# Optimization experiments

Measured on AMD Instinct MI355X. Metric: run time of the kernel, lower is better.

Reference implementation:

```python
import jax, jax.numpy as jnp
import numpy as np

N, E, F_IN, NCLS, H = 50000, 800000, 128, 10, 64


def setup_inputs() -> dict:
    key = jax.random.key(0)
    ks = jax.random.split(key, 24)
    p = lambda k, shp: (jax.random.normal(k, shp, dtype=jnp.float32) * 0.1)
    inp = {
        'x': jax.random.normal(ks[0], (N, F_IN), dtype=jnp.float32),
        'edge_index': jax.random.randint(ks[1], (2, E), 0, N, dtype=jnp.int64),
        'gcn1_W': p(ks[2], (F_IN, 128)), 'gcn1_b': p(ks[3], (128,)),
        'gcn2_W': p(ks[4], (128, 64)),  'gcn2_b': p(ks[5], (64,)),
        'gcn3_W': p(ks[6], (64, 32)),   'gcn3_b': p(ks[7], (32,)),
        'gat_W': p(ks[8], (32, 32)), 'gat_a_src': p(ks[9], (32,)),
        'gat_a_dst': p(ks[10], (32,)), 'gat_b': p(ks[11], (32,)),
        'lstm_Wih_f': p(ks[12], (4 * H, 32)), 'lstm_bih_f': p(ks[13], (4 * H,)), 'lstm_bhh_f': p(ks[14], (4 * H,)),
        'lstm_Wih_b': p(ks[15], (4 * H, 32)), 'lstm_bih_b': p(ks[16], (4 * H,)), 'lstm_bhh_b': p(ks[17], (4 * H,)),
        'bn_gamma': jnp.ones((2 * H,), jnp.float32), 'bn_beta': jnp.zeros((2 * H,), jnp.float32),
        'fc_W': p(ks[18], (NCLS, 2 * H)), 'fc_b': p(ks[19], (NCLS,)),
    }
    return inp


def _forward(x, edge_index, gcn1_W, gcn1_b, gcn2_W, gcn2_b, gcn3_W, gcn3_b,
             gat_W, gat_a_src, gat_a_dst, gat_b,
             lstm_Wih_f, lstm_bih_f, lstm_bhh_f, lstm_Wih_b, lstm_bih_b, lstm_bhh_b,
             bn_gamma, bn_beta, fc_W, fc_b):
    n = x.shape[0]
    loop = jnp.arange(n)
    row = jnp.concatenate([edge_index[0], loop])  # source nodes (+ self loops)
    col = jnp.concatenate([edge_index[1], loop])  # target nodes
    deg = jax.ops.segment_sum(jnp.ones_like(col, dtype=x.dtype), col, num_segments=n)
    dis = jax.lax.rsqrt(jnp.maximum(deg, 1e-12))  # deg >= 1 due to self loops
    norm = dis[row] * dis[col]

    def gcn(h, W, b):
        h = h @ W
        return jax.ops.segment_sum(h[row] * norm[:, None], col, num_segments=n) + b

    h = jax.nn.relu(gcn(x, gcn1_W, gcn1_b))
    h = jax.nn.relu(gcn(h, gcn2_W, gcn2_b))
    h = gcn(h, gcn3_W, gcn3_b)

    # GAT (1 head), self loops already in row/col, softmax over incoming edges per target
    g = h @ gat_W
    e = jax.nn.leaky_relu((g @ gat_a_src)[row] + (g @ gat_a_dst)[col], negative_slope=0.2)
    m = jax.ops.segment_max(e, col, num_segments=n)
    ee = jnp.exp(e - m[col])
    att = ee / jax.ops.segment_sum(ee, col, num_segments=n)[col]
    h = jax.ops.segment_sum(g[row] * att[:, None], col, num_segments=n) + gat_b
    h = jax.nn.relu(h)

    # bidirectional LSTM with seq_len=1, h0=c0=0 -> single cell step per direction
    def lstm_dir(xx, Wih, bih, bhh):
        gt = xx @ Wih.T + bih + bhh
        i, f, c, o = jnp.split(gt, 4, axis=-1)  # torch gate order i,f,g,o
        return jax.nn.sigmoid(o) * jnp.tanh(jax.nn.sigmoid(i) * jnp.tanh(c))

    r = jnp.concatenate([lstm_dir(h, lstm_Wih_f, lstm_bih_f, lstm_bhh_f),
                         lstm_dir(h, lstm_Wih_b, lstm_bih_b, lstm_bhh_b)], axis=-1)
    # eval mode: dropout = identity; BatchNorm1d with running_mean=0, running_var=1
    r = r * (bn_gamma / jnp.sqrt(jnp.float32(1.0 + 1e-5))) + bn_beta
    return r @ fc_W.T + fc_b


def reference(x, edge_index, gcn1_W, gcn1_b, gcn2_W, gcn2_b, gcn3_W, gcn3_b,
              gat_W, gat_a_src, gat_a_dst, gat_b,
              lstm_Wih_f, lstm_bih_f, lstm_bhh_f, lstm_Wih_b, lstm_bih_b, lstm_bhh_b,
              bn_gamma, bn_beta, fc_W, fc_b):
    return _forward(x, edge_index, gcn1_W, gcn1_b, gcn2_W, gcn2_b, gcn3_W, gcn3_b,
                    gat_W, gat_a_src, gat_a_dst, gat_b,
                    lstm_Wih_f, lstm_bih_f, lstm_bhh_f, lstm_Wih_b, lstm_bih_b, lstm_bhh_b,
                    bn_gamma, bn_beta, fc_W, fc_b)
```

## Files before the change

### kernel.cpp

```cpp
#include <hip/hip_runtime.h>
#include <hip/hip_bf16.h>
#include <math.h>

typedef __hip_bfloat16 bf16;

#define NN 50000
#define EE 800000
#define EPB 4096
#define NBK 196
#define BCAP 6144

__device__ __forceinline__ float b2f(bf16 v) { return __bfloat162float(v); }
__device__ __forceinline__ float rcp_(float x) { return __builtin_amdgcn_rcpf(x); }
__device__ __forceinline__ float sigmoidf_(float x) { return rcp_(1.0f + __expf(-x)); }
__device__ __forceinline__ float tanhf_(float x) {
    float xx = fminf(fmaxf(x, -15.0f), 15.0f);
    float e = __expf(2.0f * xx);
    return (e - 1.0f) * rcp_(e + 1.0f);
}
__device__ __forceinline__ float leakyf_(float x) { return x > 0.0f ? x : 0.2f * x; }
__device__ __forceinline__ unsigned short f2bf(float f) {
    unsigned u = __float_as_uint(f);
    unsigned r = (u + 0x7FFFu + ((u >> 16) & 1u)) >> 16;
    return (unsigned short)r;
}
__device__ __forceinline__ unsigned pack2(float a, float b) {
    return (unsigned)f2bf(a) | ((unsigned)f2bf(b) << 16);
}
__device__ __forceinline__ float lo_(unsigned u) { return __uint_as_float(u << 16); }
__device__ __forceinline__ float hi_(unsigned u) { return __uint_as_float(u & 0xFFFF0000u); }

#define OFF_W1 0
#define OFF_B1 16384
#define OFF_W2 16512
#define OFF_B2 24704
#define OFF_W3 24768
#define OFF_B3 26816
#define OFF_GATW 26848
#define OFF_GAS 27872
#define OFF_GAD 27904
#define OFF_GAB 27936
#define OFF_WIHF 27968
#define OFF_BIHF 36160
#define OFF_BHHF 36416
#define OFF_WIHB 36672
#define OFF_BIHB 44864
#define OFF_BHHB 45120
#define OFF_GAMMA 45376
#define OFF_BETA 45504
#define OFF_FCW 45632
#define OFF_FCB 46912
#define WTOTAL 46922

struct WSrc { const void* p[20]; };

__global__ void k_detect(const unsigned short* __restrict__ xraw,
                         const unsigned int* __restrict__ eraw, int* __restrict__ flags) {
    __shared__ int f32f, i64f;
    int t = threadIdx.x;
    if (t == 0) { f32f = 0; i64f = 1; }
    __syncthreads();
    for (int i = t; i < 4096; i += 256) {
        unsigned short u = xraw[i];
        int ex = (u >> 7) & 0xFF;
        if (ex >= 0xC0) atomicOr(&f32f, 1);
        if (eraw[2 * i + 1] != 0u) atomicAnd(&i64f, 0);
    }
    __syncthreads();
    if (t == 0) { flags[0] = f32f; flags[1] = i64f; }
}

__global__ void k_cvt_w(WSrc srcs, float* __restrict__ dst, const int* __restrict__ flags,
                        int total) {
    constexpr int WOFF[21] = {OFF_W1,   OFF_B1,   OFF_W2,   OFF_B2,   OFF_W3,   OFF_B3,
                              OFF_GATW, OFF_GAS,  OFF_GAD,  OFF_GAB,  OFF_WIHF, OFF_BIHF,
                              OFF_BHHF, OFF_WIHB, OFF_BIHB, OFF_BHHB, OFF_GAMMA, OFF_BETA,
                              OFF_FCW,  OFF_FCB,  WTOTAL};
    int i = blockIdx.x * 256 + threadIdx.x;
    if (i >= total) return;
    int tn = 0;
#pragma unroll
    for (int j = 1; j < 20; ++j)
        if (i >= WOFF[j]) tn = j;
    int local = i - WOFF[tn];
    if (flags[0]) dst[i] = ((const float*)srcs.p[tn])[local];
    else dst[i] = b2f(((const bf16*)srcs.p[tn])[local]);
}

__global__ __launch_bounds__(256) void k_hist(const void* __restrict__ eraw,
                                              unsigned* __restrict__ gh,
                                              const int* __restrict__ flags) {
    __shared__ int h[256];
    int t = threadIdx.x, b = blockIdx.x;
    h[t] = 0;
    __syncthreads();
    int e0 = b * EPB;
    bool i64 = flags[1] != 0;
    for (int i = t; i < EPB; i += 256) {
        int e = e0 + i;
        if (e < EE) {
            int d = i64 ? (int)((const long long*)eraw)[EE + e] : ((const int*)eraw)[EE + e];
            d = min(max(d, 0), NN - 1);
            atomicAdd(&h[d >> 8], 1);
        }
    }
    __syncthreads();
    gh[b * 256 + t] = (unsigned)h[t];
}

__global__ __launch_bounds__(256) void k_bscan(const unsigned* __restrict__ gh,
                                               unsigned* __restrict__ gh2,
                                               int* __restrict__ bb, int* __restrict__ rptr) {
    __shared__ int s[256];
    int t = threadIdx.x;
    unsigned run = 0;
    for (int blk = 0; blk < NBK; ++blk) {
        unsigned v = gh[blk * 256 + t];
        gh2[blk * 256 + t] = run;
        run += v;
    }
    s[t] = (int)run;
    __syncthreads();
    for (int o = 1; o < 256; o <<= 1) {
        int x = (t >= o) ? s[t - o] : 0;
        __syncthreads();
        s[t] += x;
        __syncthreads();
    }
    bb[t] = s[t] - (int)run;
    if (t == 0) rptr[NN] = EE;
}

__global__ __launch_bounds__(256) void k_scatter(const void* __restrict__ eraw,
                                                 const unsigned* __restrict__ gh2,
                                                 const int* __restrict__ bb,
                                                 int2* __restrict__ ebkt,
                                                 const int* __restrict__ flags) {
    __shared__ unsigned cur[256];
    int t = threadIdx.x, b = blockIdx.x;
    cur[t] = gh2[b * 256 + t] + (unsigned)bb[t];
    __syncthreads();
    int e0 = b * EPB;
    bool i64 = flags[1] != 0;
    for (int i = t; i < EPB; i += 256) {
        int e = e0 + i;
        if (e < EE) {
            int sn, d;
            if (i64) {
                sn = (int)((const long long*)eraw)[e];
                d = (int)((const long long*)eraw)[EE + e];
            } else {
                sn = ((const int*)eraw)[e];
                d = ((const int*)eraw)[EE + e];
            }
            sn = min(max(sn, 0), NN - 1);
            d = min(max(d, 0), NN - 1);
            unsigned pos = atomicAdd(&cur[d >> 8], 1u);
            if (pos < (unsigned)EE) ebkt[pos] = make_int2(sn, d);
        }
    }
}

__global__ __launch_bounds__(256) void k_bucket_csr(const int2* __restrict__ ebkt,
                                                    const int* __restrict__ bb,
                                                    int* __restrict__ rptr,
                                                    float* __restrict__ dis,
                                                    int* __restrict__ csr_src) {
    __shared__ int hist[256];
    __shared__ int excl[256];
    __shared__ int cur[256];
    __shared__ int sorted[BCAP];
    int t = threadIdx.x, b = blockIdx.x;
    int s0 = bb[b], s1 = bb[b + 1];
    int len = min(s1 - s0, BCAP);
    hist[t] = 0;
    __syncthreads();
    for (int i = t; i < len; i += 256) atomicAdd(&hist[ebkt[s0 + i].y & 255], 1);
    __syncthreads();
    int v = hist[t];
    excl[t] = v;
    __syncthreads();
    for (int o = 1; o < 256; o <<= 1) {
        int x = (t >= o) ? excl[t - o] : 0;
        __syncthreads();
        excl[t] += x;
        __syncthreads();
    }
    int loc = excl[t] - v;
    int node = b * 256 + t;
    if (node < NN) {
        rptr[node] = s0 + loc;
        dis[node] = rsqrtf((float)(v + 1));
    }
    cur[t] = loc;
    __syncthreads();
    for (int i = t; i < len; i += 256) {
        int2 p = ebkt[s0 + i];
        int pos = atomicAdd(&cur[p.y & 255], 1);
        if (pos < BCAP) sorted[pos] = p.x;
    }
    __syncthreads();
    for (int i = t; i < len; i += 256) csr_src[s0 + i] = sorted[i];
}

template <int KIN, int KOUT, int MODE, bool SCALE>
__global__ __launch_bounds__(256) void k_tile_mm(const void* __restrict__ A,
                                                 const float* __restrict__ W,
                                                 unsigned* __restrict__ C, int n,
                                                 const int* __restrict__ flags, int want,
                                                 const float* __restrict__ dis) {
    if (want >= 0 && flags[0] != want) return;
    constexpr int BK = 32;
    constexpr int AST = BK + 4;
    constexpr int CPT = KOUT / 16;
    __shared__ float As[64 * AST];
    __shared__ float Ws[BK * KOUT];
    int t = threadIdx.x;
    int jc = t & 15;
    int ng = t >> 4;
    int base = blockIdx.x * 64;
    float acc[4][CPT];
#pragma unroll
    for (int i = 0; i < 4; ++i)
#pragma unroll
        for (int c = 0; c < CPT; ++c) acc[i][c] = 0.f;
    int snode = t >> 2;
    int gnode = min(base + snode, n - 1);
    int koff = (t & 3) * 8;
    for (int k0 = 0; k0 < KIN; k0 += BK) {
        {
            const float4* src = (const float4*)(W + k0 * KOUT);
            float4* dst = (float4*)Ws;
#pragma unroll
            for (int p = 0; p < BK * KOUT / 1024; ++p) dst[t + p * 256] = src[t + p * 256];
        }
        if (MODE == 0) {
            const unsigned* xr = (const unsigned*)A + (size_t)gnode * (KIN / 2) + (k0 + koff) / 2;
            unsigned u0 = xr[0], u1 = xr[1], u2 = xr[2], u3 = xr[3];
            float* d = As + snode * AST + koff;
            d[0] = lo_(u0); d[1] = hi_(u0);
            d[2] = lo_(u1); d[3] = hi_(u1);
            d[4] = lo_(u2); d[5] = hi_(u2);
            d[6] = lo_(u3); d[7] = hi_(u3);
        } else {
            const float4* ar = (const float4*)((const float*)A + (size_t)gnode * KIN + k0 + koff);
            float4 v0 = ar[0], v1 = ar[1];
            float4* d = (float4*)(As + snode * AST + koff);
            d[0] = v0;
            d[1] = v1;
        }
        __syncthreads();
#pragma unroll 8
        for (int k = 0; k < BK; ++k) {
            float w[CPT];
            const float* wr = Ws + k * KOUT + jc * CPT;
            if constexpr (CPT >= 4) {
#pragma unroll
                for (int c = 0; c < CPT; c += 4) {
                    float4 wv = *(const float4*)(wr + c);
                    w[c] = wv.x; w[c + 1] = wv.y; w[c + 2] = wv.z; w[c + 3] = wv.w;
                }
            } else {
                float2 wv = *(const float2*)wr;
                w[0] = wv.x; w[1] = wv.y;
            }
            float a0 = As[(ng * 4 + 0) * AST + k];
            float a1 = As[(ng * 4 + 1) * AST + k];
            float a2 = As[(ng * 4 + 2) * AST + k];
            float a3 = As[(ng * 4 + 3) * AST + k];
#pragma unroll
            for (int c = 0; c < CPT; ++c) {
                acc[0][c] += a0 * w[c];
                acc[1][c] += a1 * w[c];
                acc[2][c] += a2 * w[c];
                acc[3][c] += a3 * w[c];
            }
        }
        __syncthreads();
    }
#pragma unroll
    for (int i = 0; i < 4; ++i) {
        int node = base + ng * 4 + i;
        if (node < n) {
            float sc = SCALE ? dis[node] : 1.0f;
            unsigned* cr = C + (size_t)node * (KOUT / 2) + jc * (CPT / 2);
#pragma unroll
            for (int c = 0; c < CPT; c += 2)
                cr[c / 2] = pack2(acc[i][c] * sc, acc[i][c + 1] * sc);
        }
    }
}

template <bool RELU>
__global__ void k_agg128(const unsigned* __restrict__ t, const int* __restrict__ rptr,
                         const int* __restrict__ csr_src, const float* __restrict__ dis,
                         const float* __restrict__ bias, float* __restrict__ out, int n) {
    int wave = (blockIdx.x * blockDim.x + threadIdx.x) >> 6;
    int lane = threadIdx.x & 63;
    if (wave >= n) return;
    int dst = wave;
    float dd = dis[dst];
    float ax, ay;
    {
        unsigned u = t[(size_t)dst * 64 + lane];
        ax = lo_(u);
        ay = hi_(u);
    }
    int s = __builtin_amdgcn_readfirstlane(max(0, min(rptr[dst], EE)));
    int e = __builtin_amdgcn_readfirstlane(max(s, min(rptr[dst + 1], EE)));
    int j = s;
    for (; j + 8 <= e; j += 8) {
        int i0 = csr_src[j], i1 = csr_src[j + 1], i2 = csr_src[j + 2], i3 = csr_src[j + 3];
        int i4 = csr_src[j + 4], i5 = csr_src[j + 5], i6 = csr_src[j + 6], i7 = csr_src[j + 7];
        unsigned u0 = t[(size_t)i0 * 64 + lane], u1 = t[(size_t)i1 * 64 + lane];
        unsigned u2 = t[(size_t)i2 * 64 + lane], u3 = t[(size_t)i3 * 64 + lane];
        unsigned u4 = t[(size_t)i4 * 64 + lane], u5 = t[(size_t)i5 * 64 + lane];
        unsigned u6 = t[(size_t)i6 * 64 + lane], u7 = t[(size_t)i7 * 64 + lane];
        ax += (lo_(u0) + lo_(u1)) + (lo_(u2) + lo_(u3)) + (lo_(u4) + lo_(u5)) + (lo_(u6) + lo_(u7));
        ay += (hi_(u0) + hi_(u1)) + (hi_(u2) + hi_(u3)) + (hi_(u4) + hi_(u5)) + (hi_(u6) + hi_(u7));
    }
    for (; j + 4 <= e; j += 4) {
        int i0 = csr_src[j], i1 = csr_src[j + 1], i2 = csr_src[j + 2], i3 = csr_src[j + 3];
        unsigned u0 = t[(size_t)i0 * 64 + lane], u1 = t[(size_t)i1 * 64 + lane];
        unsigned u2 = t[(size_t)i2 * 64 + lane], u3 = t[(size_t)i3 * 64 + lane];
        ax += (lo_(u0) + lo_(u1)) + (lo_(u2) + lo_(u3));
        ay += (hi_(u0) + hi_(u1)) + (hi_(u2) + hi_(u3));
    }
    for (; j < e; ++j) {
        unsigned u0 = t[(size_t)csr_src[j] * 64 + lane];
        ax += lo_(u0);
        ay += hi_(u0);
    }
    float2 bv = *(const float2*)(bias + 2 * lane);
    float vx = ax * dd + bv.x;
    float vy = ay * dd + bv.y;
    if (RELU) { vx = fmaxf(vx, 0.f); vy = fmaxf(vy, 0.f); }
    *(float2*)(out + (size_t)dst * 128 + 2 * lane) = make_float2(vx, vy);
}

template <bool RELU>
__global__ void k_agg64(const unsigned* __restrict__ t, const int* __restrict__ rptr,
                        const int* __restrict__ csr_src, const float* __restrict__ dis,
                        const float* __restrict__ bias, float* __restrict__ out, int n) {
    int wave = (blockIdx.x * blockDim.x + threadIdx.x) >> 6;
    int lane = threadIdx.x & 63;
    if (wave >= n) return;
    int dst = wave;
    int half = lane >> 5, l32 = lane & 31;
    float dd = dis[dst];
    float ax = 0.f, ay = 0.f;
    if (!half) {
        unsigned u = t[(size_t)dst * 32 + l32];
        ax = lo_(u);
        ay = hi_(u);
    }
    int s = max(0, min(rptr[dst], EE));
    int e = max(s, min(rptr[dst + 1], EE));
    int cnt = e - s;
    int pairs = cnt >> 1;
    int p = 0;
    for (; p + 4 <= pairs; p += 4) {
        int jb = s + 2 * p + half;
        int i0 = csr_src[jb], i1 = csr_src[jb + 2], i2 = csr_src[jb + 4], i3 = csr_src[jb + 6];
        unsigned u0 = t[(size_t)i0 * 32 + l32], u1 = t[(size_t)i1 * 32 + l32];
        unsigned u2 = t[(size_t)i2 * 32 + l32], u3 = t[(size_t)i3 * 32 + l32];
        ax += (lo_(u0) + lo_(u1)) + (lo_(u2) + lo_(u3));
        ay += (hi_(u0) + hi_(u1)) + (hi_(u2) + hi_(u3));
    }
    for (; p < pairs; ++p) {
        int i0 = csr_src[s + 2 * p + half];
        unsigned u0 = t[(size_t)i0 * 32 + l32];
        ax += lo_(u0);
        ay += hi_(u0);
    }
    if ((cnt & 1) && !half) {
        unsigned u0 = t[(size_t)csr_src[e - 1] * 32 + l32];
        ax += lo_(u0);
        ay += hi_(u0);
    }
    ax += __shfl_down(ax, 32);
    ay += __shfl_down(ay, 32);
    if (!half) {
        float2 bv = *(const float2*)(bias + 2 * l32);
        float vx = ax * dd + bv.x;
        float vy = ay * dd + bv.y;
        if (RELU) { vx = fmaxf(vx, 0.f); vy = fmaxf(vy, 0.f); }
        *(float2*)(out + (size_t)dst * 64 + 2 * l32) = make_float2(vx, vy);
    }
}

template <bool RELU>
__global__ void k_agg32(const unsigned* __restrict__ t, const int* __restrict__ rptr,
                        const int* __restrict__ csr_src, const float* __restrict__ dis,
                        const float* __restrict__ bias, float* __restrict__ out, int n) {
    int wave = (blockIdx.x * blockDim.x + threadIdx.x) >> 6;
    int lane = threadIdx.x & 63;
    if (wave >= n) return;
    int dst = wave;
    int q = lane >> 4, l16 = lane & 15;
    float dd = dis[dst];
    float ax = 0.f, ay = 0.f;
    if (q == 0) {
        unsigned u = t[(size_t)dst * 16 + l16];
        ax = lo_(u);
        ay = hi_(u);
    }
    int s = max(0, min(rptr[dst], EE));
    int e = max(s, min(rptr[dst + 1], EE));
    int cnt = e - s;
    int quads = cnt >> 2;
    int p = 0;
    for (; p + 4 <= quads; p += 4) {
        int jb = s + 4 * p + q;
        int i0 = csr_src[jb], i1 = csr_src[jb + 4], i2 = csr_src[jb + 8], i3 = csr_src[jb + 12];
        unsigned u0 = t[(size_t)i0 * 16 + l16], u1 = t[(size_t)i1 * 16 + l16];
        unsigned u2 = t[(size_t)i2 * 16 + l16], u3 = t[(size_t)i3 * 16 + l16];
        ax += (lo_(u0) + lo_(u1)) + (lo_(u2) + lo_(u3));
        ay += (hi_(u0) + hi_(u1)) + (hi_(u2) + hi_(u3));
    }
    for (; p < quads; ++p) {
        int i0 = csr_src[s + 4 * p + q];
        unsigned u0 = t[(size_t)i0 * 16 + l16];
        ax += lo_(u0);
        ay += hi_(u0);
    }
    int rem = cnt - 4 * quads;
    if (q < rem) {
        unsigned u0 = t[(size_t)csr_src[s + 4 * quads + q] * 16 + l16];
        ax += lo_(u0);
        ay += hi_(u0);
    }
    ax += __shfl_down(ax, 32);
    ay += __shfl_down(ay, 32);
    ax += __shfl_down(ax, 16);
    ay += __shfl_down(ay, 16);
    if (q == 0) {
        float2 bv = *(const float2*)(bias + 2 * l16);
        float vx = ax * dd + bv.x;
        float vy = ay * dd + bv.y;
        if (RELU) { vx = fmaxf(vx, 0.f); vy = fmaxf(vy, 0.f); }
        *(float2*)(out + (size_t)dst * 32 + 2 * l16) = make_float2(vx, vy);
    }
}

__global__ void k_gat_vec(const unsigned* __restrict__ g, const float* __restrict__ a_src,
                          const float* __restrict__ a_dst, float* __restrict__ asrc,
                          float* __restrict__ adst, int n) {
    int i = blockIdx.x * 256 + threadIdx.x;
    if (i >= n) return;
    float s = 0.0f, d = 0.0f;
    const unsigned* gr = g + (size_t)i * 16;
#pragma unroll
    for (int k = 0; k < 16; ++k) {
        unsigned u = gr[k];
        float v0 = lo_(u), v1 = hi_(u);
        s += v0 * a_src[2 * k] + v1 * a_src[2 * k + 1];
        d += v0 * a_dst[2 * k] + v1 * a_dst[2 * k + 1];
    }
    asrc[i] = s;
    adst[i] = d;
}

__global__ void k_gat_agg(const unsigned* __restrict__ g, const int* __restrict__ rptr,
                          const int* __restrict__ csr_src, const float* __restrict__ asrc,
                          const float* __restrict__ adst, const float* __restrict__ gat_b,
                          float* __restrict__ out, int n) {
    int wave = (blockIdx.x * blockDim.x + threadIdx.x) >> 6;
    int lane = threadIdx.x & 63;
    if (wave >= n) return;
    int dst = wave;
    int q = lane >> 4, l16 = lane & 15;
    float ad = adst[dst];
    int s = max(0, min(rptr[dst], EE));
    int e = max(s, min(rptr[dst + 1], EE));
    float ax = 0.f, ay = 0.f, denom = 0.f;
    if (q == 0) {
        float w0 = __expf(fminf(leakyf_(asrc[dst] + ad), 80.f));
        unsigned u = g[(size_t)dst * 16 + l16];
        ax = lo_(u) * w0;
        ay = hi_(u) * w0;
        denom = w0;
    }
    int cnt = e - s;
    int quads = cnt >> 2;
    int p = 0;
    for (; p + 4 <= quads; p += 4) {
        int jb = s + 4 * p + q;
        int i0 = csr_src[jb], i1 = csr_src[jb + 4], i2 = csr_src[jb + 8], i3 = csr_src[jb + 12];
        float a0 = asrc[i0], a1 = asrc[i1], a2 = asrc[i2], a3 = asrc[i3];
        unsigned u0 = g[(size_t)i0 * 16 + l16], u1 = g[(size_t)i1 * 16 + l16];
        unsigned u2 = g[(size_t)i2 * 16 + l16], u3 = g[(size_t)i3 * 16 + l16];
        float w0 = __expf(fminf(leakyf_(a0 + ad), 80.f));
        float w1 = __expf(fminf(leakyf_(a1 + ad), 80.f));
        float w2 = __expf(fminf(leakyf_(a2 + ad), 80.f));
        float w3 = __expf(fminf(leakyf_(a3 + ad), 80.f));
        denom += (w0 + w1) + (w2 + w3);
        ax += lo_(u0) * w0 + lo_(u1) * w1 + lo_(u2) * w2 + lo_(u3) * w3;
        ay += hi_(u0) * w0 + hi_(u1) * w1 + hi_(u2) * w2 + hi_(u3) * w3;
    }
    for (; p < quads; ++p) {
        int i0 = csr_src[s + 4 * p + q];
        float wgt = __expf(fminf(leakyf_(asrc[i0] + ad), 80.f));
        unsigned u0 = g[(size_t)i0 * 16 + l16];
        denom += wgt;
        ax += lo_(u0) * wgt;
        ay += hi_(u0) * wgt;
    }
    int rem = cnt - 4 * quads;
    if (q < rem) {
        int i0 = csr_src[s + 4 * quads + q];
        float wgt = __expf(fminf(leakyf_(asrc[i0] + ad), 80.f));
        unsigned u0 = g[(size_t)i0 * 16 + l16];
        denom += wgt;
        ax += lo_(u0) * wgt;
        ay += hi_(u0) * wgt;
    }
    ax += __shfl_down(ax, 32);
    ay += __shfl_down(ay, 32);
    denom += __shfl_down(denom, 32);
    ax += __shfl_down(ax, 16);
    ay += __shfl_down(ay, 16);
    denom += __shfl_down(denom, 16);
    if (q == 0) {
        float r = rcp_(denom);
        float vx = fmaxf(ax * r + gat_b[2 * l16], 0.f);
        float vy = fmaxf(ay * r + gat_b[2 * l16 + 1], 0.f);
        *(float2*)(out + (size_t)dst * 32 + 2 * l16) = make_float2(vx, vy);
    }
}

__global__ __launch_bounds__(256) void k_lstm_fc(const float* __restrict__ h,
                                                 const float* __restrict__ wp,
                                                 void* __restrict__ out,
                                                 const int* __restrict__ flags, int n) {
    __shared__ float ps[4 * 640];
    int t = threadIdx.x;
    int nd = t & 63;
    int part = __builtin_amdgcn_readfirstlane(t >> 6);
    int dir = part >> 1, jh = part & 1;
    int base = blockIdx.x * 64;
    int node = min(base + nd, n - 1);

    float hv[32];
    {
        const float4* hr = (const float4*)(h + (size_t)node * 32);
#pragma unroll
        for (int qq = 0; qq < 8; ++qq) {
            float4 v = hr[qq];
            hv[4 * qq + 0] = v.x;
            hv[4 * qq + 1] = v.y;
            hv[4 * qq + 2] = v.z;
            hv[4 * qq + 3] = v.w;
        }
    }

    const float* W = wp + (dir ? OFF_WIHB : OFF_WIHF);
    const float* bi = wp + (dir ? OFF_BIHB : OFF_BIHF);
    const float* bh = wp + (dir ? OFF_BHHB : OFF_BHHF);
    const float* fcw = wp + OFF_FCW;
    float p10[10];
#pragma unroll
    for (int c = 0; c < 10; ++c) p10[c] = 0.f;

    int j0 = jh * 32;
#pragma unroll 2
    for (int j = j0; j < j0 + 32; ++j) {
        const float* wi = W + (size_t)j * 32;
        const float* wc = W + (size_t)(128 + j) * 32;
        const float* wo = W + (size_t)(192 + j) * 32;
        float ai = bi[j] + bh[j];
        float ac = bi[128 + j] + bh[128 + j];
        float ao = bi[192 + j] + bh[192 + j];
#pragma unroll
        for (int k = 0; k < 32; ++k) {
            float hk = hv[k];
            ai += hk * wi[k];
            ac += hk * wc[k];
            ao += hk * wo[k];
        }
        float v = sigmoidf_(ao) * tanhf_(sigmoidf_(ai) * tanhf_(ac));
        int jj = dir * 64 + j;
        float r = v * (wp[OFF_GAMMA + jj] * rsqrtf(1.0f + 1e-5f)) + wp[OFF_BETA + jj];
#pragma unroll
        for (int c = 0; c < 10; ++c) p10[c] += r * fcw[c * 128 + jj];
    }
#pragma unroll
    for (int c = 0; c < 10; ++c) ps[part * 640 + nd * 10 + c] = p10[c];
    __syncthreads();
    bool f32o = flags[0] != 0;
    for (int idx = t; idx < 640; idx += 256) {
        int gnode = base + idx / 10;
        if (gnode < n) {
            int c = idx % 10;
            float v = wp[OFF_FCB + c] + ps[idx] + ps[640 + idx] + ps[1280 + idx] + ps[1920 + idx];
            if (f32o) ((float*)out)[(size_t)base * 10 + idx] = v;
            else ((unsigned short*)out)[(size_t)base * 10 + idx] = f2bf(v);
        }
    }
}

extern "C" void kernel_launch(void* const* d_in, const int* in_sizes, int n_in,
                              void* d_out, int out_size, void* d_ws, size_t ws_size,
                              hipStream_t stream) {
    const int N = NN;

    char* w = (char*)d_ws;
    auto alloc = [&](size_t bytes) {
        void* p = (void*)w;
        w += (bytes + 255) & ~(size_t)255;
        return p;
    };
    int* flags = (int*)alloc(256);
    float* wpool = (float*)alloc((size_t)WTOTAL * 4);
    float* dis = (float*)alloc((size_t)N * 4);
    int* rptr = (int*)alloc((size_t)(N + 1) * 4);
    int* csr_src = (int*)alloc((size_t)EE * 4);
    unsigned* gh = (unsigned*)alloc((size_t)NBK * 256 * 4);
    unsigned* gh2 = (unsigned*)alloc((size_t)NBK * 256 * 4);
    int* bb = (int*)alloc(1024);
    int2* ebkt = (int2*)alloc((size_t)EE * 8);
    float* asrc = (float*)alloc((size_t)N * 4);
    float* adst = (float*)alloc((size_t)N * 4);
    unsigned* bufT = (unsigned*)alloc((size_t)N * 64 * 4);
    float* bufH = (float*)alloc((size_t)N * 128 * 4);

    WSrc ws_srcs;
    for (int i = 0; i < 20; ++i) ws_srcs.p[i] = d_in[2 + i];

    const int NB = (N + 255) / 256;
    const int AGG = (N + 3) / 4;
    const int TMB = (N + 63) / 64;
    const int LFB = (N + 63) / 64;
    const int WB = (WTOTAL + 255) / 256;

    k_detect<<<1, 256, 0, stream>>>((const unsigned short*)d_in[0],
                                    (const unsigned int*)d_in[1], flags);
    k_cvt_w<<<WB, 256, 0, stream>>>(ws_srcs, wpool, flags, WTOTAL);
    k_hist<<<NBK, 256, 0, stream>>>(d_in[1], gh, flags);
    k_bscan<<<1, 256, 0, stream>>>(gh, gh2, bb, rptr);
    k_scatter<<<NBK, 256, 0, stream>>>(d_in[1], gh2, bb, ebkt, flags);
    k_bucket_csr<<<NBK, 256, 0, stream>>>(ebkt, bb, rptr, dis, csr_src);

    k_tile_mm<128, 128, 0, true><<<TMB, 256, 0, stream>>>(d_in[0], wpool + OFF_W1, bufT, N, flags, 0, dis);
    k_tile_mm<128, 128, 1, true><<<TMB, 256, 0, stream>>>(d_in[0], wpool + OFF_W1, bufT, N, flags, 1, dis);
    k_agg128<true><<<AGG, 256, 0, stream>>>(bufT, rptr, csr_src, dis, wpool + OFF_B1, bufH, N);
    k_tile_mm<128, 64, 1, true><<<TMB, 256, 0, stream>>>(bufH, wpool + OFF_W2, bufT, N, flags, -1, dis);
    k_agg64<true><<<AGG, 256, 0, stream>>>(bufT, rptr, csr_src, dis, wpool + OFF_B2, bufH, N);
    k_tile_mm<64, 32, 1, true><<<TMB, 256, 0, stream>>>(bufH, wpool + OFF_W3, bufT, N, flags, -1, dis);
    k_agg32<false><<<AGG, 256, 0, stream>>>(bufT, rptr, csr_src, dis, wpool + OFF_B3, bufH, N);
    k_tile_mm<32, 32, 1, false><<<TMB, 256, 0, stream>>>(bufH, wpool + OFF_GATW, bufT, N, flags, -1, dis);
    k_gat_vec<<<NB, 256, 0, stream>>>(bufT, wpool + OFF_GAS, wpool + OFF_GAD, asrc, adst, N);
    k_gat_agg<<<AGG, 256, 0, stream>>>(bufT, rptr, csr_src, asrc, adst, wpool + OFF_GAB, bufH, N);
    k_lstm_fc<<<LFB, 256, 0, stream>>>(bufH, wpool, d_out, flags, N);
}
```

Measured before the change: 382.9 us.

## Keep LSTM gate weights in registers and stage node features in LDS

The LSTM+FC kernel is restructured so each thread owns one hidden unit and holds its three 32-wide gate weight rows in registers. It then loops over 32 nodes whose features are staged in shared memory, instead of each thread owning a node and re-reading weights from global/cache every iteration. LSTM outputs go to a padded LDS tile, and a separate phase computes the FC projection. This trades many scalar weight loads for LDS broadcast reads, at the cost of higher register pressure (96 weight floats), an occupancy hint, and extra syncs.

```diff
diff --git a/kernel.cpp b/kernel.cpp
--- a/kernel.cpp
+++ b/kernel.cpp
@@ -529,63 +529,82 @@
     }
 }
 
-__global__ __launch_bounds__(256) void k_lstm_fc(const float* __restrict__ h,
-                                                 const float* __restrict__ wp,
-                                                 void* __restrict__ out,
-                                                 const int* __restrict__ flags, int n) {
+__global__ __launch_bounds__(256, 3) void k_lstm_fc(const float* __restrict__ h,
+                                                    const float* __restrict__ wp,
+                                                    void* __restrict__ out,
+                                                    const int* __restrict__ flags, int n) {
+    __shared__ float hs[64 * 32];
+    __shared__ float rs[64 * 129];
     __shared__ float ps[4 * 640];
     int t = threadIdx.x;
-    int nd = t & 63;
-    int part = __builtin_amdgcn_readfirstlane(t >> 6);
-    int dir = part >> 1, jh = part & 1;
     int base = blockIdx.x * 64;
-    int node = min(base + nd, n - 1);
-
-    float hv[32];
-    {
-        const float4* hr = (const float4*)(h + (size_t)node * 32);
-#pragma unroll
-        for (int qq = 0; qq < 8; ++qq) {
-            float4 v = hr[qq];
-            hv[4 * qq + 0] = v.x;
-            hv[4 * qq + 1] = v.y;
-            hv[4 * qq + 2] = v.z;
-            hv[4 * qq + 3] = v.w;
-        }
-    }
-
+
+    for (int i = t; i < 512; i += 256) {
+        int nd = i >> 3, k4 = i & 7;
+        int node = min(base + nd, n - 1);
+        ((float4*)hs)[i] = ((const float4*)h)[(size_t)node * 8 + k4];
+    }
+
+    int row = t & 127;
+    int grp = t >> 7;
+    int dir = row >> 6, j = row & 63;
     const float* W = wp + (dir ? OFF_WIHB : OFF_WIHF);
     const float* bi = wp + (dir ? OFF_BIHB : OFF_BIHF);
     const float* bh = wp + (dir ? OFF_BHHB : OFF_BHHF);
-    const float* fcw = wp + OFF_FCW;
-    float p10[10];
-#pragma unroll
-    for (int c = 0; c < 10; ++c) p10[c] = 0.f;
-
-    int j0 = jh * 32;
-#pragma unroll 2
-    for (int j = j0; j < j0 + 32; ++j) {
-        const float* wi = W + (size_t)j * 32;
-        const float* wc = W + (size_t)(128 + j) * 32;
-        const float* wo = W + (size_t)(192 + j) * 32;
-        float ai = bi[j] + bh[j];
-        float ac = bi[128 + j] + bh[128 + j];
-        float ao = bi[192 + j] + bh[192 + j];
+
+    float w_i[32], w_c[32], w_o[32];
+    {
+        const float4* wip = (const float4*)(W + (size_t)j * 32);
+        const float4* wcp = (const float4*)(W + (size_t)(128 + j) * 32);
+        const float4* wop = (const float4*)(W + (size_t)(192 + j) * 32);
+#pragma unroll
+        for (int k4 = 0; k4 < 8; ++k4) {
+            float4 a = wip[k4], b = wcp[k4], c = wop[k4];
+            w_i[4 * k4 + 0] = a.x; w_i[4 * k4 + 1] = a.y; w_i[4 * k4 + 2] = a.z; w_i[4 * k4 + 3] = a.w;
+            w_c[4 * k4 + 0] = b.x; w_c[4 * k4 + 1] = b.y; w_c[4 * k4 + 2] = b.z; w_c[4 * k4 + 3] = b.w;
+            w_o[4 * k4 + 0] = c.x; w_o[4 * k4 + 1] = c.y; w_o[4 * k4 + 2] = c.z; w_o[4 * k4 + 3] = c.w;
+        }
+    }
+    float bI = bi[j] + bh[j];
+    float bC = bi[128 + j] + bh[128 + j];
+    float bO = bi[192 + j] + bh[192 + j];
+    float gsc = wp[OFF_GAMMA + row] * rsqrtf(1.0f + 1e-5f);
+    float gbe = wp[OFF_BETA + row];
+
+    __syncthreads();
+
+    int slot0 = grp * 32;
+    for (int nn = 0; nn < 32; ++nn) {
+        const float* hvp = hs + (slot0 + nn) * 32;
+        float ai = bI, ac = bC, ao = bO;
 #pragma unroll
         for (int k = 0; k < 32; ++k) {
-            float hk = hv[k];
-            ai += hk * wi[k];
-            ac += hk * wc[k];
-            ao += hk * wo[k];
+            float hk = hvp[k];
+            ai += hk * w_i[k];
+            ac += hk * w_c[k];
+            ao += hk * w_o[k];
         }
         float v = sigmoidf_(ao) * tanhf_(sigmoidf_(ai) * tanhf_(ac));
-        int jj = dir * 64 + j;
-        float r = v * (wp[OFF_GAMMA + jj] * rsqrtf(1.0f + 1e-5f)) + wp[OFF_BETA + jj];
-#pragma unroll
-        for (int c = 0; c < 10; ++c) p10[c] += r * fcw[c * 128 + jj];
-    }
-#pragma unroll
-    for (int c = 0; c < 10; ++c) ps[part * 640 + nd * 10 + c] = p10[c];
+        rs[(slot0 + nn) * 129 + row] = v * gsc + gbe;
+    }
+    __syncthreads();
+
+    {
+        int nd = t & 63, quarter = t >> 6;
+        const float* fcw = wp + OFF_FCW;
+        int jbase = quarter * 32;
+        float p10[10];
+#pragma unroll
+        for (int c = 0; c < 10; ++c) p10[c] = 0.f;
+#pragma unroll 4
+        for (int k = 0; k < 32; ++k) {
+            float r = rs[nd * 129 + jbase + k];
+#pragma unroll
+            for (int c = 0; c < 10; ++c) p10[c] += r * fcw[c * 128 + jbase + k];
+        }
+#pragma unroll
+        for (int c = 0; c < 10; ++c) ps[quarter * 640 + nd * 10 + c] = p10[c];
+    }
     __syncthreads();
     bool f32o = flags[0] != 0;
     for (int idx = t; idx < 640; idx += 256) {
```

Measured after the change: 375.6 us. About the same (-1.9%).
